# Performance work log

Measured on AMD Instinct MI355X. Metric: run time of the kernel, lower is better.

## Reference

```python
import jax, jax.numpy as jnp
import numpy as np

FEATS = 768
HEAD = 12
HD = FEATS // HEAD


def setup_inputs() -> dict:
    key = jax.random.key(0)
    ks = jax.random.split(key, 10)
    b, n, f = 8, 1024, FEATS
    s = 1.0 / np.sqrt(f)
    return {
        "x": jax.random.normal(ks[0], (b, n, f), dtype=jnp.float32),
        "bias": jnp.zeros((), dtype=jnp.float32),
        "Wq": jax.random.normal(ks[1], (f, f), dtype=jnp.float32) * s,
        "bq": jnp.zeros((f,), dtype=jnp.float32),
        "Wk": jax.random.normal(ks[2], (f, f), dtype=jnp.float32) * s,
        "bk": jnp.zeros((f,), dtype=jnp.float32),
        "Wv": jax.random.normal(ks[3], (f, f), dtype=jnp.float32) * s,
        "bv": jnp.zeros((f,), dtype=jnp.float32),
        "Wo": jax.random.normal(ks[4], (f, f), dtype=jnp.float32) * s,
        "bo": jnp.zeros((f,), dtype=jnp.float32),
    }


def reference(x, bias, Wq, bq, Wk, bk, Wv, bv, Wo, bo):
    b, n, f = x.shape
    sqrt_d = jnp.sqrt(jnp.asarray(f, dtype=x.dtype))  # scale uses full feats, per source

    def split_heads(t):  # (b,n,f) -> (b,h,n,hd)
        return t.reshape(b, n, HEAD, HD).transpose(0, 2, 1, 3)

    q = split_heads(x @ Wq.T + bq)
    k = split_heads(x @ Wk.T + bk)
    v = split_heads(x @ Wv.T + bv)

    # sigmoid attention: no row-wise normalization
    score = jax.nn.sigmoid(jnp.einsum('bhif,bhjf->bhij', q, k) / sqrt_d + bias)
    attn = jnp.einsum('bhij,bhjf->bihf', score, v)  # (b,n,h,hd)
    o = attn.reshape(b, n, f) @ Wo.T + bo  # dropout p=0.0 -> identity
    return o
```

## Files before the change

### kernel.cpp

```cpp
#include <hip/hip_runtime.h>

#define FEATS 768
#define NHEAD 12
#define HD    64
#define SEQ   1024
#define NB    8
#define MROWS (NB*SEQ)
#define NQK   (2*FEATS)
#define QKVN  (3*FEATS)
#define QSC   0.0520616136f

typedef __attribute__((ext_vector_type(8))) __bf16          bf16x8;
typedef __attribute__((ext_vector_type(4))) __bf16          bf16x4;
typedef __attribute__((ext_vector_type(4))) unsigned short  us4;
typedef __attribute__((ext_vector_type(4))) float           f32x4;

__device__ __forceinline__ unsigned short f2bf(float f) {
  union { float f; unsigned u; } v; v.f = f;
  return (unsigned short)((v.u + 0x7fffu + ((v.u >> 16) & 1u)) >> 16);
}

__device__ __forceinline__ void gload_lds16(const void* g, void* l) {
  __builtin_amdgcn_global_load_lds(
      (const __attribute__((address_space(1))) void*)g,
      (__attribute__((address_space(3))) void*)l, 16, 0, 0);
}

__global__ void cast_all(const float* __restrict__ x,
                         const float* __restrict__ Wq, const float* __restrict__ Wk,
                         const float* __restrict__ Wv, const float* __restrict__ Wo,
                         const float* __restrict__ bq, const float* __restrict__ bk,
                         const float* __restrict__ bv,
                         unsigned short* __restrict__ Xbf,
                         unsigned short* __restrict__ Wcat,
                         unsigned short* __restrict__ Wobf,
                         float* __restrict__ bcat) {
  int blk = blockIdx.x;
  if (blk < 6144) {
    int i = blk * 256 + threadIdx.x;
    f32x4 v = ((const f32x4*)x)[i];
    us4 o;
    o[0] = f2bf(v[0]); o[1] = f2bf(v[1]); o[2] = f2bf(v[2]); o[3] = f2bf(v[3]);
    ((us4*)Xbf)[i] = o;
  } else if (blk < 8448) {
    int bb = blk - 6144;
    int mtx = bb / 576;
    int i = (bb % 576) * 256 + threadIdx.x;
    const float* src = (mtx == 0) ? Wq : (mtx == 1) ? Wk : (mtx == 2) ? Wv : Wo;
    f32x4 v = ((const f32x4*)src)[i];
    us4 o;
    o[0] = f2bf(v[0]); o[1] = f2bf(v[1]); o[2] = f2bf(v[2]); o[3] = f2bf(v[3]);
    if (mtx < 3) ((us4*)Wcat)[mtx * 147456 + i] = o;
    else         ((us4*)Wobf)[i] = o;
  } else {
    int i = (blk - 8448) * 256 + threadIdx.x;
    if (i < QKVN)
      bcat[i] = (i < FEATS) ? bq[i] : (i < 2*FEATS ? bk[i-FEATS] : bv[i-2*FEATS]);
  }
}

#define FOFF(row) ((row)*64 + (((g) ^ (((row) >> 1) & 3)) << 4))

__global__ __launch_bounds__(256, 3) void gemm1_bt(
    const unsigned short* __restrict__ A,
    const unsigned short* __restrict__ B,
    const float* __restrict__ bias,
    unsigned short* __restrict__ QKo,
    unsigned short* __restrict__ VTo)
{
  __shared__ __align__(16) char Al[2 * 8192];
  __shared__ __align__(16) char Bl[3 * 12288];

  const int tid  = threadIdx.x;
  const int lane = tid & 63;
  const int w    = tid >> 6;
  const int l15  = lane & 15;
  const int g    = lane >> 4;
  const int wm   = (w >> 1) * 64;
  const int wn   = (w & 1) * 96;

  const int id  = blockIdx.x;
  const int xcd = id & 7;
  const int j   = id >> 3;
  const int mi  = xcd * 8 + (j & 7);
  const int ni  = j >> 3;
  const int mbase = mi * 128;
  const int nbase = ni * 192;

  const int trow  = tid >> 2;
  const int sslot = ((tid & 3) ^ ((tid >> 3) & 3)) * 8;
  const unsigned short* Ag = A + (size_t)(mbase + trow) * 768 + sslot;
  const unsigned short* Bg = B + (size_t)(nbase + trow) * 768 + sslot;

  auto STAGE_A = [&](int buf, int t) {
    const unsigned short* sa = Ag + t * 32;
    char* da = Al + buf * 8192 + tid * 16;
    gload_lds16(sa,            da);
    gload_lds16(sa + 64*768,   da + 4096);
  };
  auto STAGE_B = [&](int buf, int t) {
    const unsigned short* sb = Bg + t * 32;
    char* db = Bl + buf * 12288 + tid * 16;
    gload_lds16(sb,            db);
    gload_lds16(sb + 64*768,   db + 4096);
    gload_lds16(sb + 128*768,  db + 8192);
  };

  f32x4 acc[4][6] = {};

  STAGE_A(0, 0);
  STAGE_B(0, 0);
  STAGE_B(1, 1);
  asm volatile("s_waitcnt vmcnt(3)" ::: "memory");
  __builtin_amdgcn_s_barrier();

  for (int t = 0; t < 24; t++) {
    if (t < 23) STAGE_A((t + 1) & 1, t + 1);
    if (t < 22) STAGE_B((t + 2) % 3, t + 2);

    const char* Ab = Al + (t & 1) * 8192;
    const char* Bb = Bl + (t % 3) * 12288;
    bf16x8 af[4];
#pragma unroll
    for (int mf = 0; mf < 4; mf++) {
      const int row = wm + mf*16 + l15;
      af[mf] = *(const bf16x8*)(Ab + FOFF(row));
    }
    __builtin_amdgcn_s_setprio(1);
#pragma unroll
    for (int nf = 0; nf < 6; nf++) {
      const int row = wn + nf*16 + l15;
      bf16x8 bfv = *(const bf16x8*)(Bb + FOFF(row));
#pragma unroll
      for (int mf = 0; mf < 4; mf++)
        acc[mf][nf] = __builtin_amdgcn_mfma_f32_16x16x32_bf16(af[mf], bfv, acc[mf][nf], 0, 0, 0);
    }
    __builtin_amdgcn_s_setprio(0);

    if (t < 23) {
      if (t < 22) asm volatile("s_waitcnt vmcnt(3)" ::: "memory");
      else        asm volatile("s_waitcnt vmcnt(0)" ::: "memory");
      __builtin_amdgcn_s_barrier();
    }
  }

  const bool isQK = (ni < 8);
  const float osc = (ni < 4) ? QSC : 1.0f;
#pragma unroll
  for (int mf = 0; mf < 4; mf++)
#pragma unroll
    for (int nf = 0; nf < 6; nf++) {
      const int col  = nbase + wn + nf*16 + l15;
      const float bb = bias[col];
      const int row0 = mbase + wm + mf*16 + g*4;
      if (isQK) {
#pragma unroll
        for (int r = 0; r < 4; r++)
          QKo[(size_t)(row0 + r)*NQK + col] = f2bf((acc[mf][nf][r] + bb) * osc);
      } else {
        const int c  = col - NQK;
        const int hh = c >> 6, dd = c & 63;
        const int bI = row0 >> 10, n0 = row0 & 1023;
        const int rl  = n0 & 63;
        const int cp  = ((rl >> 5) << 5) | (((rl >> 2) & 3) << 3) | (((rl >> 4) & 1) << 2);
        const int n0p = (n0 & ~63) | cp;
        us4 o;
#pragma unroll
        for (int r = 0; r < 4; r++) o[r] = f2bf(acc[mf][nf][r] + bb);
        *(us4*)(VTo + ((size_t)((bI*NHEAD + hh)*HD + dd))*SEQ + n0p) = o;
      }
    }
}

__global__ __launch_bounds__(256, 4) void gemm2_bt(
    const unsigned short* __restrict__ A,
    const unsigned short* __restrict__ B,
    const float* __restrict__ bias,
    float* __restrict__ C)
{
  __shared__ __align__(16) char Al[2 * 4096];
  __shared__ __align__(16) char Bl[3 * 8192];

  const int tid  = threadIdx.x;
  const int lane = tid & 63;
  const int w    = tid >> 6;
  const int l15  = lane & 15;
  const int g    = lane >> 4;
  const int wm   = (w >> 1) * 32;
  const int wn   = (w & 1) * 64;

  const int id  = blockIdx.x;
  const int xcd = id & 7;
  const int j   = id >> 3;
  const int mi  = xcd * 16 + (j & 15);
  const int ni  = j >> 4;
  const int mbase = mi * 64;
  const int nbase = ni * 128;

  const int trow  = tid >> 2;
  const int sslot = ((tid & 3) ^ ((tid >> 3) & 3)) * 8;
  const unsigned short* Ag = A + (size_t)(mbase + trow) * 768 + sslot;
  const unsigned short* Bg = B + (size_t)(nbase + trow) * 768 + sslot;

  auto STAGE_A = [&](int buf, int t) {
    char* da = Al + buf * 4096 + tid * 16;
    gload_lds16(Ag + t * 32, da);
  };
  auto STAGE_B = [&](int buf, int t) {
    const unsigned short* sb = Bg + t * 32;
    char* db = Bl + buf * 8192 + tid * 16;
    gload_lds16(sb,           db);
    gload_lds16(sb + 64*768,  db + 4096);
  };

  f32x4 acc[2][4] = {};

  STAGE_A(0, 0);
  STAGE_B(0, 0);
  STAGE_B(1, 1);
  asm volatile("s_waitcnt vmcnt(2)" ::: "memory");
  __builtin_amdgcn_s_barrier();

  for (int t = 0; t < 24; t++) {
    if (t < 23) STAGE_A((t + 1) & 1, t + 1);
    if (t < 22) STAGE_B((t + 2) % 3, t + 2);

    const char* Ab = Al + (t & 1) * 4096;
    const char* Bb = Bl + (t % 3) * 8192;
    bf16x8 af[2], bfv[4];
#pragma unroll
    for (int mf = 0; mf < 2; mf++) {
      const int row = wm + mf*16 + l15;
      af[mf] = *(const bf16x8*)(Ab + FOFF(row));
    }
#pragma unroll
    for (int nf = 0; nf < 4; nf++) {
      const int row = wn + nf*16 + l15;
      bfv[nf] = *(const bf16x8*)(Bb + FOFF(row));
    }
    __builtin_amdgcn_s_setprio(1);
#pragma unroll
    for (int mf = 0; mf < 2; mf++)
#pragma unroll
      for (int nf = 0; nf < 4; nf++)
        acc[mf][nf] = __builtin_amdgcn_mfma_f32_16x16x32_bf16(af[mf], bfv[nf], acc[mf][nf], 0, 0, 0);
    __builtin_amdgcn_s_setprio(0);

    if (t < 23) {
      if (t < 22) asm volatile("s_waitcnt vmcnt(2)" ::: "memory");
      else        asm volatile("s_waitcnt vmcnt(0)" ::: "memory");
      __builtin_amdgcn_s_barrier();
    }
  }

#pragma unroll
  for (int mf = 0; mf < 2; mf++)
#pragma unroll
    for (int nf = 0; nf < 4; nf++) {
      const int col  = nbase + wn + nf*16 + l15;
      const float bb = bias[col];
      const int row0 = mbase + wm + mf*16 + g*4;
#pragma unroll
      for (int r = 0; r < 4; r++)
        C[(size_t)(row0 + r)*FEATS + col] = acc[mf][nf][r] + bb;
    }
}
#undef FOFF

__global__ __launch_bounds__(256, 3) void attn_kernel(
    const unsigned short* __restrict__ QK,
    const unsigned short* __restrict__ VT,
    const float* __restrict__ biasp,
    unsigned short* __restrict__ AO)
{
  __shared__ __align__(16) char Kl[2][8192];
  __shared__ __align__(16) char Vl[2][8192];

  const int tid  = threadIdx.x;
  const int lane = tid & 63;
  const int w    = tid >> 6;
  const int l15  = lane & 15;
  const int g    = lane >> 4;

  const int id  = blockIdx.x;
  const int r8  = id & 7;
  const int m   = id >> 3;
  const int bh  = r8 * 12 + (m >> 3);
  const int qx  = m & 7;
  const int b   = bh / NHEAD;
  const int h   = bh % NHEAD;
  const int rowB  = b * SEQ;
  const int qbase = rowB + qx * 128;

  const float Kb = __builtin_amdgcn_exp2f(-biasp[0] * 1.4426950408889634f);

  bf16x8 qf[2][2];
  {
    const unsigned short* qp = QK + (size_t)(qbase + w*32 + l15) * NQK + h*HD + g*8;
    qf[0][0] = *(const bf16x8*)(qp);
    qf[0][1] = *(const bf16x8*)(qp + 32);
    qf[1][0] = *(const bf16x8*)(qp + 16*NQK);
    qf[1][1] = *(const bf16x8*)(qp + 16*NQK + 32);
  }

  const int trow = tid >> 3;
  const int colb = ((tid & 7) * 16) ^ ((trow & 7) << 4);
  const char* Ksrc = (const char*)QK +
      ((size_t)(rowB + trow) * NQK + FEATS + h*HD) * 2 + colb;
  const char* Vsrc = (const char*)VT +
      ((size_t)(bh*HD + trow)) * (SEQ*2) + colb;

  auto STAGE_K = [&](int p, int t) {
    char* kw = Kl[p] + tid*16;
    gload_lds16(Ksrc + (size_t)t * 64 * (NQK*2),              kw);
    gload_lds16(Ksrc + (size_t)t * 64 * (NQK*2) + 32*(NQK*2), kw + 4096);
  };
  auto STAGE_V = [&](int p, int t) {
    char* vw = Vl[p] + tid*16;
    gload_lds16(Vsrc + t * 128,              vw);
    gload_lds16(Vsrc + t * 128 + 32*(SEQ*2), vw + 4096);
  };

  f32x4 o_acc[4][2] = {};
  f32x4 sE[2][4], sO[2][4];

  auto SIGPV = [&](f32x4 (&sP)[2][4], const char* Vp) {
    bf16x8 paq[2][2];
#pragma unroll
    for (int qm = 0; qm < 2; qm++) {
      float sg[4][4];
#pragma unroll
      for (int nf = 0; nf < 4; nf++)
#pragma unroll
        for (int rr = 0; rr < 4; rr++) {
          const float e = __builtin_amdgcn_exp2f(-sP[qm][nf][rr]);
          sg[nf][rr] = __builtin_amdgcn_rcpf(__builtin_fmaf(Kb, e, 1.0f));
        }
#pragma unroll
      for (int js = 0; js < 2; js++) {
        bf16x8 pa;
#pragma unroll
        for (int jj = 0; jj < 4; jj++) {
          pa[jj]     = (__bf16)sg[2*js][jj];
          pa[jj + 4] = (__bf16)sg[2*js + 1][jj];
        }
        paq[qm][js] = pa;
      }
    }
#pragma unroll
    for (int js = 0; js < 2; js++) {
      bf16x8 vf[4];
#pragma unroll
      for (int df = 0; df < 4; df++) {
        const int row = df*16 + l15;
        const int by  = (row*128 + js*64 + g*16) ^ ((row & 7) << 4);
        vf[df] = *(const bf16x8*)(Vp + by);
      }
      __builtin_amdgcn_s_setprio(1);
#pragma unroll
      for (int df = 0; df < 4; df++)
#pragma unroll
        for (int qm = 0; qm < 2; qm++)
          o_acc[df][qm] = __builtin_amdgcn_mfma_f32_16x16x32_bf16(vf[df], paq[qm][js], o_acc[df][qm], 0, 0, 0);
      __builtin_amdgcn_s_setprio(0);
    }
  };

  auto BODY = [&](int t, f32x4 (&sC)[2][4], f32x4 (&sP)[2][4], bool stK, bool doPrev) {
    if (stK) STAGE_K((t + 1) & 1, t + 1);
    STAGE_V(t & 1, t);

    const char* Kp = Kl[t & 1];
#pragma unroll
    for (int qm = 0; qm < 2; qm++)
#pragma unroll
      for (int nf = 0; nf < 4; nf++)
        sC[qm][nf] = (f32x4){0.f, 0.f, 0.f, 0.f};
    __builtin_amdgcn_s_setprio(1);
#pragma unroll
    for (int nf = 0; nf < 4; nf++)
#pragma unroll
      for (int ks = 0; ks < 2; ks++) {
        const int row = nf*16 + l15;
        const int by  = (row*128 + ks*64 + g*16) ^ ((row & 7) << 4);
        bf16x8 kf = *(const bf16x8*)(Kp + by);
        sC[0][nf] = __builtin_amdgcn_mfma_f32_16x16x32_bf16(kf, qf[0][ks], sC[0][nf], 0, 0, 0);
        sC[1][nf] = __builtin_amdgcn_mfma_f32_16x16x32_bf16(kf, qf[1][ks], sC[1][nf], 0, 0, 0);
      }
    __builtin_amdgcn_s_setprio(0);

    if (doPrev) SIGPV(sP, Vl[(t - 1) & 1]);

    __syncthreads();
  };

  STAGE_K(0, 0);
  __syncthreads();

  BODY(0, sE, sO, true, false);
#pragma unroll 1
  for (int t = 1; t < 15; t += 2) {
    BODY(t,     sO, sE, true, true);
    BODY(t + 1, sE, sO, true, true);
  }
  BODY(15, sO, sE, false, true);
  SIGPV(sO, Vl[1]);

  unsigned short* aop = AO + (size_t)(qbase + w*32) * FEATS + h*HD;
#pragma unroll
  for (int df = 0; df < 4; df++)
#pragma unroll
    for (int qm = 0; qm < 2; qm++) {
      const int q  = qm*16 + l15;
      const int d0 = df*16 + g*4;
      bf16x4 o;
#pragma unroll
      for (int rr = 0; rr < 4; rr++) o[rr] = (__bf16)o_acc[df][qm][rr];
      *(bf16x4*)(aop + (size_t)q * FEATS + d0) = o;
    }
}

extern "C" void kernel_launch(void* const* d_in, const int* in_sizes, int n_in,
                              void* d_out, int out_size, void* d_ws, size_t ws_size,
                              hipStream_t stream) {
  const float* x    = (const float*)d_in[0];
  const float* bias = (const float*)d_in[1];
  const float* Wq   = (const float*)d_in[2];
  const float* bq   = (const float*)d_in[3];
  const float* Wk   = (const float*)d_in[4];
  const float* bk   = (const float*)d_in[5];
  const float* Wv   = (const float*)d_in[6];
  const float* bv   = (const float*)d_in[7];
  const float* Wo   = (const float*)d_in[8];
  const float* bo   = (const float*)d_in[9];
  float* out = (float*)d_out;

  char* ws = (char*)d_ws;
  unsigned short* Xbf  = (unsigned short*)(ws + 0);
  unsigned short* Wcat = (unsigned short*)(ws + 12582912);
  unsigned short* Wobf = (unsigned short*)(ws + 16121856);
  float*          bcat = (float*)        (ws + 17301504);
  unsigned short* QKb  = (unsigned short*)(ws + 17310720);
  unsigned short* VTb  = (unsigned short*)(ws + 42476544);
  unsigned short* AO   = Xbf;

  cast_all<<<8457, 256, 0, stream>>>(x, Wq, Wk, Wv, Wo, bq, bk, bv,
                                     Xbf, Wcat, Wobf, bcat);

  gemm1_bt<<<768, 256, 0, stream>>>(Xbf, Wcat, bcat, QKb, VTb);

  attn_kernel<<<768, 256, 0, stream>>>(QKb, VTb, bias, AO);

  gemm2_bt<<<768, 256, 0, stream>>>(AO, Wobf, bo, out);
}
```

Before: 105.1 us.

## Fuse fp32-to-bf16 cast of x into the QKV GEMM A-tile staging

The separate elementwise pass that turned x into bf16 is removed. The QKV GEMM now reads fp32 x straight into registers, converts it to bf16, and writes it into the swizzled LDS A buffer. This avoids a full read and write of the activation tensor in global memory. In exchange, A staging becomes a synchronous register path instead of async global-to-LDS loads, gemm1 reads twice as many A bytes per tile, and the loop adds extra waitcnts and register pressure.

New measurement: 105.0 us, median of 2. Within noise of the previous version (-0.0%).

```diff
diff --git a/kernel.cpp b/kernel.cpp
--- a/kernel.cpp
+++ b/kernel.cpp
@@ -26,26 +26,17 @@
       (__attribute__((address_space(3))) void*)l, 16, 0, 0);
 }
 
-__global__ void cast_all(const float* __restrict__ x,
-                         const float* __restrict__ Wq, const float* __restrict__ Wk,
+__global__ void cast_all(const float* __restrict__ Wq, const float* __restrict__ Wk,
                          const float* __restrict__ Wv, const float* __restrict__ Wo,
                          const float* __restrict__ bq, const float* __restrict__ bk,
                          const float* __restrict__ bv,
-                         unsigned short* __restrict__ Xbf,
                          unsigned short* __restrict__ Wcat,
                          unsigned short* __restrict__ Wobf,
                          float* __restrict__ bcat) {
   int blk = blockIdx.x;
-  if (blk < 6144) {
-    int i = blk * 256 + threadIdx.x;
-    f32x4 v = ((const f32x4*)x)[i];
-    us4 o;
-    o[0] = f2bf(v[0]); o[1] = f2bf(v[1]); o[2] = f2bf(v[2]); o[3] = f2bf(v[3]);
-    ((us4*)Xbf)[i] = o;
-  } else if (blk < 8448) {
-    int bb = blk - 6144;
-    int mtx = bb / 576;
-    int i = (bb % 576) * 256 + threadIdx.x;
+  if (blk < 2304) {
+    int mtx = blk / 576;
+    int i = (blk % 576) * 256 + threadIdx.x;
     const float* src = (mtx == 0) ? Wq : (mtx == 1) ? Wk : (mtx == 2) ? Wv : Wo;
     f32x4 v = ((const f32x4*)src)[i];
     us4 o;
@@ -53,7 +44,7 @@
     if (mtx < 3) ((us4*)Wcat)[mtx * 147456 + i] = o;
     else         ((us4*)Wobf)[i] = o;
   } else {
-    int i = (blk - 8448) * 256 + threadIdx.x;
+    int i = (blk - 2304) * 256 + threadIdx.x;
     if (i < QKVN)
       bcat[i] = (i < FEATS) ? bq[i] : (i < 2*FEATS ? bk[i-FEATS] : bv[i-2*FEATS]);
   }
@@ -62,7 +53,7 @@
 #define FOFF(row) ((row)*64 + (((g) ^ (((row) >> 1) & 3)) << 4))
 
 __global__ __launch_bounds__(256, 3) void gemm1_bt(
-    const unsigned short* __restrict__ A,
+    const float* __restrict__ X,
     const unsigned short* __restrict__ B,
     const float* __restrict__ bias,
     unsigned short* __restrict__ QKo,
@@ -89,14 +80,33 @@
 
   const int trow  = tid >> 2;
   const int sslot = ((tid & 3) ^ ((tid >> 3) & 3)) * 8;
-  const unsigned short* Ag = A + (size_t)(mbase + trow) * 768 + sslot;
+  const float*          Ag = X + (size_t)(mbase + trow) * 768 + sslot;
   const unsigned short* Bg = B + (size_t)(nbase + trow) * 768 + sslot;
 
-  auto STAGE_A = [&](int buf, int t) {
-    const unsigned short* sa = Ag + t * 32;
+  f32x4 ar[4];
+
+  auto LOAD_A = [&](int t) {
+    const float* sa = Ag + t * 32;
+    ar[0] = *(const f32x4*)(sa);
+    ar[1] = *(const f32x4*)(sa + 4);
+    ar[2] = *(const f32x4*)(sa + 64*768);
+    ar[3] = *(const f32x4*)(sa + 64*768 + 4);
+  };
+  auto WRITE_A = [&](int buf) {
     char* da = Al + buf * 8192 + tid * 16;
-    gload_lds16(sa,            da);
-    gload_lds16(sa + 64*768,   da + 4096);
+    us4 o0, o1;
+#pragma unroll
+    for (int k = 0; k < 4; k++) { o0[k] = f2bf(ar[0][k]); }
+#pragma unroll
+    for (int k = 0; k < 4; k++) { o1[k] = f2bf(ar[1][k]); }
+    *(us4*)(da)     = o0;
+    *(us4*)(da + 8) = o1;
+#pragma unroll
+    for (int k = 0; k < 4; k++) { o0[k] = f2bf(ar[2][k]); }
+#pragma unroll
+    for (int k = 0; k < 4; k++) { o1[k] = f2bf(ar[3][k]); }
+    *(us4*)(da + 4096)     = o0;
+    *(us4*)(da + 4096 + 8) = o1;
   };
   auto STAGE_B = [&](int buf, int t) {
     const unsigned short* sb = Bg + t * 32;
@@ -108,14 +118,16 @@
 
   f32x4 acc[4][6] = {};
 
-  STAGE_A(0, 0);
+  LOAD_A(0);
   STAGE_B(0, 0);
   STAGE_B(1, 1);
+  WRITE_A(0);
   asm volatile("s_waitcnt vmcnt(3)" ::: "memory");
+  asm volatile("s_waitcnt lgkmcnt(0)" ::: "memory");
   __builtin_amdgcn_s_barrier();
 
   for (int t = 0; t < 24; t++) {
-    if (t < 23) STAGE_A((t + 1) & 1, t + 1);
+    if (t < 23) LOAD_A(t + 1);
     if (t < 22) STAGE_B((t + 2) % 3, t + 2);
 
     const char* Ab = Al + (t & 1) * 8192;
@@ -138,8 +150,9 @@
     __builtin_amdgcn_s_setprio(0);
 
     if (t < 23) {
-      if (t < 22) asm volatile("s_waitcnt vmcnt(3)" ::: "memory");
-      else        asm volatile("s_waitcnt vmcnt(0)" ::: "memory");
+      WRITE_A((t + 1) & 1);
+      asm volatile("s_waitcnt vmcnt(3)" ::: "memory");
+      asm volatile("s_waitcnt lgkmcnt(0)" ::: "memory");
       __builtin_amdgcn_s_barrier();
     }
   }
@@ -444,10 +457,10 @@
   unsigned short* VTb  = (unsigned short*)(ws + 42476544);
   unsigned short* AO   = Xbf;
 
-  cast_all<<<8457, 256, 0, stream>>>(x, Wq, Wk, Wv, Wo, bq, bk, bv,
-                                     Xbf, Wcat, Wobf, bcat);
-
-  gemm1_bt<<<768, 256, 0, stream>>>(Xbf, Wcat, bcat, QKb, VTb);
+  cast_all<<<2313, 256, 0, stream>>>(Wq, Wk, Wv, Wo, bq, bk, bv,
+                                     Wcat, Wobf, bcat);
+
+  gemm1_bt<<<768, 256, 0, stream>>>(x, Wcat, bcat, QKb, VTb);
 
   attn_kernel<<<768, 256, 0, stream>>>(QKb, VTb, bias, AO);
 
```
